# Optimization experiments

Hardware: AMD Instinct MI355X
Metric: run time of the kernel (lower is better)

The kernel has to match this reference:

```python
import jax, jax.numpy as jnp
import numpy as np

HIDDEN = 4096
NUM_HEADS = 32
NUM_KV_HEADS = 8
HEAD_DIM = HIDDEN // NUM_HEADS  # 128
Q_SIZE = NUM_HEADS * HEAD_DIM    # 4096
KV_SIZE = NUM_KV_HEADS * HEAD_DIM  # 1024
SCALE = 1.0 / HEAD_DIM  # attention_multiplier=None -> head_dim ** (-1)
ROPE_BASE = 10000.0


def _rope_neox(x, positions):
    # x: [B, S, H, D], positions: [B, S] int
    half = HEAD_DIM // 2
    inv_freq = 1.0 / (ROPE_BASE ** (jnp.arange(0, half, dtype=jnp.float32) / half))
    freqs = positions.astype(jnp.float32)[..., None] * inv_freq  # [B, S, half]
    cos = jnp.cos(freqs)[:, :, None, :]  # [B, S, 1, half]
    sin = jnp.sin(freqs)[:, :, None, :]
    x1, x2 = x[..., :half], x[..., half:]
    return jnp.concatenate([x1 * cos - x2 * sin, x2 * cos + x1 * sin], axis=-1)


def setup_inputs() -> dict:
    key = jax.random.key(0)
    k1, k2, k3 = jax.random.split(key, 3)
    B, S = 2, 2048
    positions = jnp.broadcast_to(jnp.arange(S, dtype=jnp.int32), (B, S))
    hidden_states = jax.random.normal(k1, (B, S, HIDDEN), dtype=jnp.float32) * 0.02
    w_qkv = jax.random.normal(k2, (Q_SIZE + 2 * KV_SIZE, HIDDEN), dtype=jnp.float32) * 0.02
    w_o = jax.random.normal(k3, (HIDDEN, Q_SIZE), dtype=jnp.float32) * 0.02
    return {"positions": positions, "hidden_states": hidden_states, "w_qkv": w_qkv, "w_o": w_o}


def reference(positions, hidden_states, w_qkv, w_o):
    B, S, _ = hidden_states.shape
    # fused QKV projection
    qkv = jnp.einsum('bsh,oh->bso', hidden_states, w_qkv)
    q = qkv[..., :Q_SIZE].reshape(B, S, NUM_HEADS, HEAD_DIM)
    k = qkv[..., Q_SIZE:Q_SIZE + KV_SIZE].reshape(B, S, NUM_KV_HEADS, HEAD_DIM)
    v = qkv[..., Q_SIZE + KV_SIZE:].reshape(B, S, NUM_KV_HEADS, HEAD_DIM)
    # neox-style RoPE on q and k
    q = _rope_neox(q, positions)
    k = _rope_neox(k, positions)
    # GQA: repeat kv heads
    rep = NUM_HEADS // NUM_KV_HEADS
    k = jnp.repeat(k, rep, axis=2)  # [B, S, NUM_HEADS, D]
    v = jnp.repeat(v, rep, axis=2)
    # causal attention
    scores = jnp.einsum('bqhd,bkhd->bhqk', q, k) * SCALE
    causal = jnp.tril(jnp.ones((S, S), dtype=bool))
    scores = jnp.where(causal, scores, jnp.finfo(scores.dtype).min)
    probs = jax.nn.softmax(scores, axis=-1)
    attn = jnp.einsum('bhqk,bkhd->bqhd', probs, v).reshape(B, S, Q_SIZE)
    # output projection
    return jnp.einsum('bsq,hq->bsh', attn, w_o)
```

## Files before the change

kernel.cpp:

```cpp
#include <hip/hip_runtime.h>
#include <hip/hip_bf16.h>
#include <cmath>

typedef __bf16 bf16x8 __attribute__((ext_vector_type(8)));
typedef __bf16 bf16x4 __attribute__((ext_vector_type(4)));
typedef float  f32x4  __attribute__((ext_vector_type(4)));
typedef unsigned int u32;
typedef u32 u32x4 __attribute__((ext_vector_type(4)));

#define AS1 __attribute__((address_space(1)))
#define AS3 __attribute__((address_space(3)))
#define GLDS16(gp, lp) __builtin_amdgcn_global_load_lds((AS1 void*)(gp), (AS3 void*)(lp), 16, 0, 0)

#define B_DIM 2
#define S_LEN 2048
#define HIDDEN 4096
#define NHEADS 32
#define NKV 8
#define HDIM 128
#define QSZ 4096
#define KVSZ 1024
#define QKVSZ 6144
#define GK 4096
#define ATT_SCALE 0.0078125f
#define L2E 1.4426950408889634f

__global__ __launch_bounds__(256) void conv3_f32_bf16(const float* __restrict__ i0, __bf16* __restrict__ o0, int n0,
                                                      const float* __restrict__ i1, __bf16* __restrict__ o1, int n1,
                                                      const float* __restrict__ i2, __bf16* __restrict__ o2, int n2) {
    const int total = n0 + n1 + n2;
    for (int idx = blockIdx.x * 256 + threadIdx.x; idx < total; idx += gridDim.x * 256) {
        const float* in; __bf16* out; int j = idx;
        if (j < n0) { in = i0; out = o0; }
        else if ((j -= n0) < n1) { in = i1; out = o1; }
        else { j -= n1; in = i2; out = o2; }
        float4 v = ((const float4*)in)[j];
        bf16x4 o;
        o[0] = (__bf16)v.x; o[1] = (__bf16)v.y; o[2] = (__bf16)v.z; o[3] = (__bf16)v.w;
        ((bf16x4*)out)[j] = o;
    }
}

__global__ __launch_bounds__(256) void rope_table_kernel(float* __restrict__ ct,
                                                         float* __restrict__ st) {
    int idx = blockIdx.x * 256 + threadIdx.x;
    int p = idx >> 6, i = idx & 63;
    float inv = expf(-(float)i * (9.210340371976184f / 64.0f));
    float freq = (float)p * inv;
    float s, c;
    sincosf(freq, &s, &c);
    ct[idx] = c; st[idx] = s;
}

template<typename OUT, bool VDIR>
__global__ __launch_bounds__(512, 2) void gemm256(const __bf16* __restrict__ A,
                                                  const __bf16* __restrict__ B,
                                                  OUT* __restrict__ C,
                                                  __bf16* __restrict__ Vt,
                                                  int N) {
    __shared__ __bf16 Asm[2 * 16384 + 2 * 16384];
    char* Bbase = (char*)Asm + 65536;

    const int tid = threadIdx.x;
    const int w = tid >> 6, l = tid & 63;
    const int l15 = l & 15, l4 = l >> 4;
    const int wr = w >> 2, wc = w & 3;

    const int nwg = gridDim.x * gridDim.y;
    const int orig = blockIdx.y * gridDim.x + blockIdx.x;
    const int swz = (orig & 7) * (nwg >> 3) + (orig >> 3);
    const int bx = swz % gridDim.x, by = swz / gridDim.x;
    const int m0 = by * 256, n0 = bx * 256;

    const __bf16* Ag = A + (size_t)m0 * GK;
    const __bf16* Bg = B + (size_t)n0 * GK;

#define STAGE_AQ(q, tile) do {                                                  \
        int c_ = (q) * 512 + tid;                                               \
        int r_ = c_ >> 3;                                                       \
        int jg_ = (tid & 7) ^ (r_ & 7);                                         \
        GLDS16(Ag + (size_t)r_ * GK + (tile) * 64 + jg_ * 8,                    \
               (char*)Asm + ((tile) & 1) * 32768 + c_ * 16);                    \
    } while (0)
#define STAGE_BS(s, tile) do {                                                  \
        _Pragma("unroll")                                                       \
        for (int i_ = 0; i_ < 2; ++i_) {                                        \
            int v_ = i_ * 512 + tid;                                            \
            int r_ = (v_ >> 8) * 64 + (s) * 32 + ((v_ >> 3) & 31);              \
            int jg_ = (v_ & 7) ^ (r_ & 7);                                      \
            int c_ = r_ * 8 + (v_ & 7);                                         \
            GLDS16(Bg + (size_t)r_ * GK + (tile) * 64 + jg_ * 8,                \
                   Bbase + ((tile) & 1) * 32768 + c_ * 16);                     \
        }                                                                       \
    } while (0)

#define LOAD_A(DST, MH) do {                                                    \
        _Pragma("unroll")                                                       \
        for (int m2 = 0; m2 < 4; ++m2) {                                        \
            int row = wr * 128 + ((MH) * 4 + m2) * 16 + l15;                    \
            _Pragma("unroll")                                                   \
            for (int kk = 0; kk < 2; ++kk) {                                    \
                int j = (kk * 4 + l4) ^ (row & 7);                              \
                DST[m2][kk] = *(const bf16x8*)(Als + row * 64 + j * 8);         \
            }                                                                   \
        }                                                                       \
    } while (0)
#define LOAD_B(DST, NH) do {                                                    \
        _Pragma("unroll")                                                       \
        for (int n2 = 0; n2 < 2; ++n2) {                                        \
            int row = wc * 64 + ((NH) * 2 + n2) * 16 + l15;                     \
            _Pragma("unroll")                                                   \
            for (int kk = 0; kk < 2; ++kk) {                                    \
                int j = (kk * 4 + l4) ^ (row & 7);                              \
                DST[n2][kk] = *(const bf16x8*)(Bls + row * 64 + j * 8);         \
            }                                                                   \
        }                                                                       \
    } while (0)
#define MFMA_QUAD(AF, BF, MI0, NI0)                                             \
    _Pragma("unroll")                                                           \
    for (int m2 = 0; m2 < 4; ++m2)                                              \
        _Pragma("unroll")                                                       \
        for (int n2 = 0; n2 < 2; ++n2)                                          \
            _Pragma("unroll")                                                   \
            for (int kk = 0; kk < 2; ++kk)                                      \
                acc[(MI0) + m2][(NI0) + n2] =                                   \
                    __builtin_amdgcn_mfma_f32_16x16x32_bf16(                    \
                        AF[m2][kk], BF[n2][kk], acc[(MI0) + m2][(NI0) + n2], 0, 0, 0);

    f32x4 acc[8][4] = {};

    const int T = GK / 64;
    STAGE_AQ(0, 0); STAGE_AQ(1, 0); STAGE_AQ(2, 0); STAGE_AQ(3, 0);
    STAGE_BS(0, 0); STAGE_BS(1, 0);
    STAGE_AQ(0, 1); STAGE_AQ(2, 1); STAGE_BS(0, 1);
    asm volatile("s_waitcnt vmcnt(4)" ::: "memory");
    __builtin_amdgcn_s_barrier();

    for (int t = 0; t < T; ++t) {
        const __bf16* Als = Asm + (t & 1) * 16384;
        const __bf16* Bls = (__bf16*)Bbase + (t & 1) * 16384;
        bf16x8 af0[4][2], af1[4][2], bA[2][2], bB[2][2];
        LOAD_A(af0, 0);
        LOAD_B(bA, 0);
        if (t + 1 < T) { STAGE_AQ(1, t + 1); STAGE_AQ(3, t + 1); }
        __builtin_amdgcn_s_barrier();
        __builtin_amdgcn_s_setprio(1);
        MFMA_QUAD(af0, bA, 0, 0);
        __builtin_amdgcn_s_setprio(0);
        __builtin_amdgcn_s_barrier();
        LOAD_B(bB, 1);
        if (t + 1 < T) STAGE_BS(1, t + 1);
        __builtin_amdgcn_s_barrier();
        __builtin_amdgcn_s_setprio(1);
        MFMA_QUAD(af0, bB, 0, 2);
        __builtin_amdgcn_s_setprio(0);
        __builtin_amdgcn_s_barrier();
        LOAD_A(af1, 1);
        if (t + 2 < T) { STAGE_AQ(0, t + 2); STAGE_AQ(2, t + 2); }
        __builtin_amdgcn_s_barrier();
        __builtin_amdgcn_s_setprio(1);
        MFMA_QUAD(af1, bA, 4, 0);
        __builtin_amdgcn_s_setprio(0);
        __builtin_amdgcn_s_barrier();
        if (t + 2 < T) STAGE_BS(0, t + 2);
        __builtin_amdgcn_s_barrier();
        __builtin_amdgcn_s_setprio(1);
        MFMA_QUAD(af1, bB, 4, 2);
        __builtin_amdgcn_s_setprio(0);
        if (t + 2 < T)      { asm volatile("s_waitcnt vmcnt(4)" ::: "memory"); }
        else if (t + 1 < T) { asm volatile("s_waitcnt vmcnt(0)" ::: "memory"); }
        __builtin_amdgcn_s_barrier();
    }
#undef MFMA_QUAD
#undef LOAD_A
#undef LOAD_B
#undef STAGE_AQ
#undef STAGE_BS

    if (VDIR && n0 >= QSZ + KVSZ) {
#pragma unroll
        for (int mi = 0; mi < 8; ++mi) {
            int s0 = m0 + wr * 128 + mi * 16 + l4 * 4;
            int b = s0 >> 11, s = s0 & 2047;
#pragma unroll
            for (int ni = 0; ni < 4; ++ni) {
                int vcol = n0 - (QSZ + KVSZ) + wc * 64 + ni * 16 + l15;
                int g = vcol >> 7, d = vcol & 127;
                bf16x4 o4;
#pragma unroll
                for (int r = 0; r < 4; ++r) o4[r] = (__bf16)acc[mi][ni][r];
                *(bf16x4*)(Vt + ((size_t)((b * 8 + g) * HDIM + d)) * S_LEN + s) = o4;
            }
        }
    } else {
#pragma unroll
        for (int mi = 0; mi < 8; ++mi)
#pragma unroll
            for (int ni = 0; ni < 4; ++ni)
#pragma unroll
                for (int r = 0; r < 4; ++r)
                    C[(size_t)(m0 + wr * 128 + mi * 16 + l4 * 4 + r) * N
                      + n0 + wc * 64 + ni * 16 + l15] = (OUT)acc[mi][ni][r];
    }
}

__global__ __launch_bounds__(256) void rope_kernel(const __bf16* __restrict__ qkv,
                                                   const int* __restrict__ pos,
                                                   const float* __restrict__ ct,
                                                   const float* __restrict__ st,
                                                   __bf16* __restrict__ Qb,
                                                   __bf16* __restrict__ Kb) {
    const int tid = threadIdx.x;
    const int tok = blockIdx.x;
    const int b = tok >> 11, s = tok & 2047;
    const int p = pos[tok];
    const __bf16* base = qkv + (size_t)tok * QKVSZ;
    const float* cb = ct + (size_t)p * 64;
    const float* sb = st + (size_t)p * 64;
    for (int u = tid; u < 640; u += 256) {
        int head = u >> 4, i = (u & 15) * 4;
        float4 c4 = *(const float4*)(cb + i);
        float4 s4 = *(const float4*)(sb + i);
        const bool isQ = (head < 32);
        const __bf16* src = base + (isQ ? head * HDIM : QSZ + (head - 32) * HDIM);
        bf16x4 x1 = *(const bf16x4*)(src + i);
        bf16x4 x2 = *(const bf16x4*)(src + 64 + i);
        float c[4] = {c4.x, c4.y, c4.z, c4.w};
        float sn[4] = {s4.x, s4.y, s4.z, s4.w};
        bf16x4 o1, o2;
        if (isQ) {
#pragma unroll
            for (int k = 0; k < 4; ++k) {
                float a = (float)x1[k], bv = (float)x2[k];
                o1[k] = (__bf16)((a * c[k] - bv * sn[k]) * ATT_SCALE);
                o2[k] = (__bf16)((bv * c[k] + a * sn[k]) * ATT_SCALE);
            }
            size_t o = ((size_t)(b * 32 + head) * S_LEN + s) * HDIM + i;
            *(bf16x4*)(Qb + o)      = o1;
            *(bf16x4*)(Qb + o + 64) = o2;
        } else {
#pragma unroll
            for (int k = 0; k < 4; ++k) {
                float a = (float)x1[k], bv = (float)x2[k];
                o1[k] = (__bf16)(a * c[k] - bv * sn[k]);
                o2[k] = (__bf16)(bv * c[k] + a * sn[k]);
            }
            int g = head - 32;
            size_t o = ((size_t)(b * 8 + g) * S_LEN + s) * HDIM + i;
            *(bf16x4*)(Kb + o)      = o1;
            *(bf16x4*)(Kb + o + 64) = o2;
        }
    }
}

__global__ __launch_bounds__(512, 2) void attn_kernel(const __bf16* __restrict__ Q,
                                                      const __bf16* __restrict__ K,
                                                      const __bf16* __restrict__ Vt,
                                                      __bf16* __restrict__ O) {
    const int tid = threadIdx.x;
    const int w = tid >> 6, l = tid & 63;
    const int l15 = l & 15, l4 = l >> 4;
    const int flat = blockIdx.x + (blockIdx.y << 2) + (blockIdx.z << 7);
    const int swz = (flat & 7) * 32 + (flat >> 3);
    const int p = swz & 3;
    const int hb = swz >> 2;
    const int h = hb & 31, b = hb >> 5;
    const int g = h >> 2;

    __shared__ __bf16 Ks[4][64 * 128];
    __shared__ __bf16 Vs[4][128 * 64];

    const __bf16* Kp = K + (size_t)(b * 8 + g) * S_LEN * HDIM;
    const __bf16* Vp = Vt + (size_t)(b * 8 + g) * HDIM * S_LEN;

#define RED16(x, OPINS) do {                                                      \
        u32 ra_ = __builtin_bit_cast(u32, x), rb_;                                \
        asm("v_mov_b32 %0, %1" : "=v"(rb_) : "v"(ra_));                           \
        asm("v_permlane16_swap_b32 %0, %1" : "+v"(ra_), "+v"(rb_));               \
        x = OPINS(__builtin_bit_cast(float, ra_), __builtin_bit_cast(float, rb_));\
    } while (0)
#define RED32(x, OPINS) do {                                                      \
        u32 ra_ = __builtin_bit_cast(u32, x), rb_;                                \
        asm("v_mov_b32 %0, %1" : "=v"(rb_) : "v"(ra_));                           \
        asm("v_permlane32_swap_b32 %0, %1" : "+v"(ra_), "+v"(rb_));               \
        x = OPINS(__builtin_bit_cast(float, ra_), __builtin_bit_cast(float, rb_));\
    } while (0)
#define FADD_(a_, b_) ((a_) + (b_))

#define STAGE(ktile) do {                                                          \
        const int buf_ = (ktile) & 3;                                              \
        const __bf16* kbase = Kp + (size_t)(ktile) * 64 * HDIM;                    \
        _Pragma("unroll")                                                          \
        for (int i_ = 0; i_ < 2; ++i_) {                                           \
            int c_ = i_ * 512 + tid;                \
            int row_ = c_ >> 4, cc_ = (c_ & 15) ^ (row_ & 7);                      \
            GLDS16(kbase + (size_t)row_ * HDIM + cc_ * 8,                          \
                   (char*)Ks[buf_] + c_ * 16);                                     \
        }                                                                          \
        const __bf16* vbase = Vp + (size_t)(ktile) * 64;                           \
        _Pragma("unroll")                                                          \
        for (int i_ = 0; i_ < 2; ++i_) {                                           \
            int c_ = i_ * 512 + tid;                \
            int row_ = c_ >> 3, cc_ = (c_ & 7) ^ (row_ & 7);                       \
            GLDS16(vbase + (size_t)row_ * S_LEN + cc_ * 8,                         \
                   (char*)Vs[buf_] + c_ * 16);                                     \
        }                                                                          \
    } while (0)

    for (int pi = 0; pi < 2; ++pi) {
        const int qt = pi ? (7 - p) : p;
        const int qw0 = qt * 256 + w * 32;
        const __bf16* Qp = Q + ((size_t)((b * 32 + h) * S_LEN + qw0)) * HDIM;

        bf16x8 qf[2][4];
#pragma unroll
        for (int qh = 0; qh < 2; ++qh)
#pragma unroll
            for (int kk = 0; kk < 4; ++kk)
                qf[qh][kk] = *(const bf16x8*)(Qp + (size_t)(qh * 16 + l15) * HDIM + kk * 32 + l4 * 8);

        f32x4 acc[2][8] = {};
        float m[2]    = {-1e30f, -1e30f};
        float lsum[2] = {0.f, 0.f};

        const int nkt = 4 * qt + 4;
        if (pi) { asm volatile("s_waitcnt vmcnt(0)" ::: "memory"); }
        STAGE(0);
        STAGE(1);
        STAGE(2);

        for (int kt = 0; kt < nkt; ++kt) {
            if (kt + 3 < nkt) STAGE(kt + 3);
            {
                int rem = nkt - 1 - kt;
                if (rem >= 3)      { asm volatile("s_waitcnt vmcnt(12)" ::: "memory"); }
                else if (rem == 2) { asm volatile("s_waitcnt vmcnt(8)"  ::: "memory"); }
                else if (rem == 1) { asm volatile("s_waitcnt vmcnt(4)"  ::: "memory"); }
                else               { asm volatile("s_waitcnt vmcnt(0)"  ::: "memory"); }
            }
            __builtin_amdgcn_sched_barrier(0);
            __builtin_amdgcn_s_barrier();
            __builtin_amdgcn_sched_barrier(0);
            const int cur = kt & 3;
            if (kt * 64 <= qw0 + 31) {
                f32x4 sfr[2][4];
                __builtin_amdgcn_s_setprio(1);
#pragma unroll
                for (int fn = 0; fn < 4; ++fn) {
                    f32x4 sa0 = {}, sa1 = {};
#pragma unroll
                    for (int kk = 0; kk < 4; ++kk) {
                        int row = fn * 16 + l15;
                        int cc = (kk * 4 + l4) ^ (l15 & 7);
                        bf16x8 kb = *(const bf16x8*)(Ks[cur] + row * HDIM + cc * 8);
                        sa0 = __builtin_amdgcn_mfma_f32_16x16x32_bf16(kb, qf[0][kk], sa0, 0, 0, 0);
                        sa1 = __builtin_amdgcn_mfma_f32_16x16x32_bf16(kb, qf[1][kk], sa1, 0, 0, 0);
                    }
                    sfr[0][fn] = sa0; sfr[1][fn] = sa1;
                }
                __builtin_amdgcn_s_setprio(0);
                const bool needmask = (kt * 64 + 63 > qw0);
                bf16x8 pb[2][2];
#pragma unroll
                for (int qh = 0; qh < 2; ++qh) {
                    const int qrow = qw0 + qh * 16 + l15;
                    float pmax = -1e30f;
#pragma unroll
                    for (int fn = 0; fn < 4; ++fn)
#pragma unroll
                        for (int r = 0; r < 4; ++r) {
                            float v = sfr[qh][fn][r];
                            if (needmask) {
                                int kcol = kt * 64 + fn * 16 + l4 * 4 + r;
                                if (kcol > qrow) v = -1e30f;
                            }
                            sfr[qh][fn][r] = v;
                            pmax = fmaxf(pmax, v);
                        }
                    RED16(pmax, fmaxf);
                    RED32(pmax, fmaxf);
                    if (!__all(pmax - m[qh] <= 8.0f)) {
                        float mn = fmaxf(m[qh], pmax);
                        float alpha = exp2f((m[qh] - mn) * L2E);
                        m[qh] = mn;
                        lsum[qh] *= alpha;
#pragma unroll
                        for (int n = 0; n < 8; ++n)
#pragma unroll
                            for (int r = 0; r < 4; ++r) acc[qh][n][r] *= alpha;
                    }
                    float rs = 0.f;
                    u32 pk01[4], pk23[4];
#pragma unroll
                    for (int fn = 0; fn < 4; ++fn) {
                        float p0 = exp2f((sfr[qh][fn][0] - m[qh]) * L2E);
                        float p1 = exp2f((sfr[qh][fn][1] - m[qh]) * L2E);
                        float p2 = exp2f((sfr[qh][fn][2] - m[qh]) * L2E);
                        float p3 = exp2f((sfr[qh][fn][3] - m[qh]) * L2E);
                        rs += (p0 + p1) + (p2 + p3);
                        asm("v_cvt_pk_bf16_f32 %0, %1, %2" : "=v"(pk01[fn]) : "v"(p0), "v"(p1));
                        asm("v_cvt_pk_bf16_f32 %0, %1, %2" : "=v"(pk23[fn]) : "v"(p2), "v"(p3));
                    }
                    RED16(rs, FADD_);
                    RED32(rs, FADD_);
                    lsum[qh] += rs;
#pragma unroll
                    for (int kk = 0; kk < 2; ++kk) {
                        u32 w0 = pk01[2 * kk], w2 = pk01[2 * kk + 1];
                        asm("v_permlane32_swap_b32 %0, %1" : "+v"(w0), "+v"(w2));
                        asm("v_permlane16_swap_b32 %0, %1" : "+v"(w0), "+v"(w2));
                        u32 w1 = pk23[2 * kk], w3 = pk23[2 * kk + 1];
                        asm("v_permlane32_swap_b32 %0, %1" : "+v"(w1), "+v"(w3));
                        asm("v_permlane16_swap_b32 %0, %1" : "+v"(w1), "+v"(w3));
                        u32x4 wv;
                        wv[0] = w0; wv[1] = w1; wv[2] = w2; wv[3] = w3;
                        pb[qh][kk] = __builtin_bit_cast(bf16x8, wv);
                    }
                }
                __builtin_amdgcn_s_setprio(1);
#pragma unroll
                for (int kk = 0; kk < 2; ++kk) {
#pragma unroll
                    for (int n = 0; n < 8; ++n) {
                        int row = n * 16 + l15;
                        int cc = (kk * 4 + l4) ^ (l15 & 7);
                        bf16x8 vb = *(const bf16x8*)(Vs[cur] + row * 64 + cc * 8);
                        acc[0][n] = __builtin_amdgcn_mfma_f32_16x16x32_bf16(vb, pb[0][kk], acc[0][n], 0, 0, 0);
                        acc[1][n] = __builtin_amdgcn_mfma_f32_16x16x32_bf16(vb, pb[1][kk], acc[1][n], 0, 0, 0);
                    }
                }
                __builtin_amdgcn_s_setprio(0);
            }
            __builtin_amdgcn_sched_barrier(0);
            __builtin_amdgcn_s_barrier();
            __builtin_amdgcn_sched_barrier(0);
        }
#pragma unroll
        for (int qh = 0; qh < 2; ++qh) {
            float inv = 1.0f / lsum[qh];
            int qrow = qw0 + qh * 16 + l15;
            __bf16* obase = O + ((size_t)(b * S_LEN) + qrow) * QSZ + h * HDIM + l4 * 4;
#pragma unroll
            for (int n = 0; n < 8; ++n) {
                bf16x4 o4;
#pragma unroll
                for (int r = 0; r < 4; ++r) o4[r] = (__bf16)(acc[qh][n][r] * inv);
                *(bf16x4*)(obase + n * 16) = o4;
            }
        }
    }
#undef STAGE
#undef RED16
#undef RED32
#undef FADD_
}

extern "C" void kernel_launch(void* const* d_in, const int* in_sizes, int n_in,
                              void* d_out, int out_size, void* d_ws, size_t ws_size,
                              hipStream_t stream) {
    const int*   pos    = (const int*)d_in[0];
    const float* hidden = (const float*)d_in[1];
    const float* wqkv   = (const float*)d_in[2];
    const float* wo     = (const float*)d_in[3];
    float* out = (float*)d_out;

    __bf16* hb    = (__bf16*)d_ws;
    __bf16* wqb   = hb  + 16777216;
    __bf16* wob   = wqb + 25165824;
    __bf16* qkv   = wob + 16777216;
    __bf16* Qb    = qkv + 25165824;
    __bf16* Kb    = Qb  + 16777216;
    __bf16* Vtb   = Kb  + 4194304;
    __bf16* attnb = Vtb + 4194304;
    float*  rc    = (float*)(attnb + 16777216);
    float*  rs    = rc + 131072;

    conv3_f32_bf16<<<2048, 256, 0, stream>>>(hidden, hb, 4194304,
                                             wqkv, wqb, 6291456,
                                             wo, wob, 4194304);
    rope_table_kernel<<<512, 256, 0, stream>>>(rc, rs);
    gemm256<__bf16, true><<<dim3(QKVSZ / 256, (B_DIM * S_LEN) / 256), 512, 0, stream>>>(
        hb, wqb, qkv, Vtb, QKVSZ);
    rope_kernel<<<B_DIM * S_LEN, 256, 0, stream>>>(qkv, pos, rc, rs, Qb, Kb);
    attn_kernel<<<dim3(4, NHEADS, B_DIM), 512, 0, stream>>>(Qb, Kb, Vtb, attnb);
    gemm256<float, false><<<dim3(HIDDEN / 256, (B_DIM * S_LEN) / 256), 512, 0, stream>>>(
        attnb, wob, out, nullptr, HIDDEN);
}
```

Measured before the change: 515.0 us.

## Fuse RoPE into QKV GEMM epilogue via LDS staging, drop separate rope kernel

The QKV GEMM epilogue now stages the Q/K output tile through shared memory as bf16, then applies neox RoPE (with attention scale for Q) and writes directly to the head-major Q and K buffers. The standalone rope kernel and the intermediate qkv buffer are removed. This avoids a kernel launch and a full write-then-read of the QKV activations. In exchange the GEMM epilogue gets extra LDS traffic and barriers plus gathered cos/sin table loads.

```diff
diff --git a/kernel.cpp b/kernel.cpp
--- a/kernel.cpp
+++ b/kernel.cpp
@@ -52,11 +52,16 @@
     ct[idx] = c; st[idx] = s;
 }
 
-template<typename OUT, bool VDIR>
+template<typename OUT, int MODE>
 __global__ __launch_bounds__(512, 2) void gemm256(const __bf16* __restrict__ A,
                                                   const __bf16* __restrict__ B,
                                                   OUT* __restrict__ C,
                                                   __bf16* __restrict__ Vt,
+                                                  __bf16* __restrict__ Qb,
+                                                  __bf16* __restrict__ Kb,
+                                                  const int* __restrict__ pos,
+                                                  const float* __restrict__ ct,
+                                                  const float* __restrict__ st,
                                                   int N) {
     __shared__ __bf16 Asm[2 * 16384 + 2 * 16384];
     char* Bbase = (char*)Asm + 65536;
@@ -177,19 +182,74 @@
 #undef STAGE_AQ
 #undef STAGE_BS
 
-    if (VDIR && n0 >= QSZ + KVSZ) {
-#pragma unroll
-        for (int mi = 0; mi < 8; ++mi) {
-            int s0 = m0 + wr * 128 + mi * 16 + l4 * 4;
-            int b = s0 >> 11, s = s0 & 2047;
-#pragma unroll
-            for (int ni = 0; ni < 4; ++ni) {
-                int vcol = n0 - (QSZ + KVSZ) + wc * 64 + ni * 16 + l15;
-                int g = vcol >> 7, d = vcol & 127;
-                bf16x4 o4;
-#pragma unroll
-                for (int r = 0; r < 4; ++r) o4[r] = (__bf16)acc[mi][ni][r];
-                *(bf16x4*)(Vt + ((size_t)((b * 8 + g) * HDIM + d)) * S_LEN + s) = o4;
+    if (MODE == 1) {
+        if (n0 >= QSZ + KVSZ) {
+#pragma unroll
+            for (int mi = 0; mi < 8; ++mi) {
+                int s0 = m0 + wr * 128 + mi * 16 + l4 * 4;
+                int b = s0 >> 11, s = s0 & 2047;
+#pragma unroll
+                for (int ni = 0; ni < 4; ++ni) {
+                    int vcol = n0 - (QSZ + KVSZ) + wc * 64 + ni * 16 + l15;
+                    int g = vcol >> 7, d = vcol & 127;
+                    bf16x4 o4;
+#pragma unroll
+                    for (int r = 0; r < 4; ++r) o4[r] = (__bf16)acc[mi][ni][r];
+                    *(bf16x4*)(Vt + ((size_t)((b * 8 + g) * HDIM + d)) * S_LEN + s) = o4;
+                }
+            }
+        } else {
+            __bf16* X = (__bf16*)Asm;
+            __syncthreads();
+#pragma unroll
+            for (int mi = 0; mi < 8; ++mi)
+#pragma unroll
+                for (int ni = 0; ni < 4; ++ni)
+#pragma unroll
+                    for (int r = 0; r < 4; ++r)
+                        X[(wr * 128 + mi * 16 + l4 * 4 + r) * 256
+                          + wc * 64 + ni * 16 + l15] = (__bf16)acc[mi][ni][r];
+            __syncthreads();
+            const bool isQ = (n0 < QSZ);
+#pragma unroll
+            for (int it = 0; it < 16; ++it) {
+                int idx = it * 512 + tid;
+                int q4 = (idx & 15) * 4;
+                int hh = (idx >> 4) & 1;
+                int lt = idx >> 5;
+                int tok = m0 + lt;
+                int bb = tok >> 11, ss = tok & 2047;
+                int pp = pos[tok];
+                float4 c4 = *(const float4*)(ct + (size_t)pp * 64 + q4);
+                float4 s4 = *(const float4*)(st + (size_t)pp * 64 + q4);
+                bf16x4 x1 = *(const bf16x4*)(X + lt * 256 + hh * 128 + q4);
+                bf16x4 x2 = *(const bf16x4*)(X + lt * 256 + hh * 128 + 64 + q4);
+                float cc[4] = {c4.x, c4.y, c4.z, c4.w};
+                float sn[4] = {s4.x, s4.y, s4.z, s4.w};
+                bf16x4 o1, o2;
+                if (isQ) {
+#pragma unroll
+                    for (int k = 0; k < 4; ++k) {
+                        float a = (float)x1[k], bv = (float)x2[k];
+                        o1[k] = (__bf16)((a * cc[k] - bv * sn[k]) * ATT_SCALE);
+                        o2[k] = (__bf16)((bv * cc[k] + a * sn[k]) * ATT_SCALE);
+                    }
+                    int gh = (n0 >> 7) + hh;
+                    size_t o = ((size_t)(bb * 32 + gh) * S_LEN + ss) * HDIM + q4;
+                    *(bf16x4*)(Qb + o)      = o1;
+                    *(bf16x4*)(Qb + o + 64) = o2;
+                } else {
+#pragma unroll
+                    for (int k = 0; k < 4; ++k) {
+                        float a = (float)x1[k], bv = (float)x2[k];
+                        o1[k] = (__bf16)(a * cc[k] - bv * sn[k]);
+                        o2[k] = (__bf16)(bv * cc[k] + a * sn[k]);
+                    }
+                    int gk = ((n0 - QSZ) >> 7) + hh;
+                    size_t o = ((size_t)(bb * 8 + gk) * S_LEN + ss) * HDIM + q4;
+                    *(bf16x4*)(Kb + o)      = o1;
+                    *(bf16x4*)(Kb + o + 64) = o2;
+                }
             }
         }
     } else {
@@ -201,55 +261,6 @@
                 for (int r = 0; r < 4; ++r)
                     C[(size_t)(m0 + wr * 128 + mi * 16 + l4 * 4 + r) * N
                       + n0 + wc * 64 + ni * 16 + l15] = (OUT)acc[mi][ni][r];
-    }
-}
-
-__global__ __launch_bounds__(256) void rope_kernel(const __bf16* __restrict__ qkv,
-                                                   const int* __restrict__ pos,
-                                                   const float* __restrict__ ct,
-                                                   const float* __restrict__ st,
-                                                   __bf16* __restrict__ Qb,
-                                                   __bf16* __restrict__ Kb) {
-    const int tid = threadIdx.x;
-    const int tok = blockIdx.x;
-    const int b = tok >> 11, s = tok & 2047;
-    const int p = pos[tok];
-    const __bf16* base = qkv + (size_t)tok * QKVSZ;
-    const float* cb = ct + (size_t)p * 64;
-    const float* sb = st + (size_t)p * 64;
-    for (int u = tid; u < 640; u += 256) {
-        int head = u >> 4, i = (u & 15) * 4;
-        float4 c4 = *(const float4*)(cb + i);
-        float4 s4 = *(const float4*)(sb + i);
-        const bool isQ = (head < 32);
-        const __bf16* src = base + (isQ ? head * HDIM : QSZ + (head - 32) * HDIM);
-        bf16x4 x1 = *(const bf16x4*)(src + i);
-        bf16x4 x2 = *(const bf16x4*)(src + 64 + i);
-        float c[4] = {c4.x, c4.y, c4.z, c4.w};
-        float sn[4] = {s4.x, s4.y, s4.z, s4.w};
-        bf16x4 o1, o2;
-        if (isQ) {
-#pragma unroll
-            for (int k = 0; k < 4; ++k) {
-                float a = (float)x1[k], bv = (float)x2[k];
-                o1[k] = (__bf16)((a * c[k] - bv * sn[k]) * ATT_SCALE);
-                o2[k] = (__bf16)((bv * c[k] + a * sn[k]) * ATT_SCALE);
-            }
-            size_t o = ((size_t)(b * 32 + head) * S_LEN + s) * HDIM + i;
-            *(bf16x4*)(Qb + o)      = o1;
-            *(bf16x4*)(Qb + o + 64) = o2;
-        } else {
-#pragma unroll
-            for (int k = 0; k < 4; ++k) {
-                float a = (float)x1[k], bv = (float)x2[k];
-                o1[k] = (__bf16)(a * c[k] - bv * sn[k]);
-                o2[k] = (__bf16)(bv * c[k] + a * sn[k]);
-            }
-            int g = head - 32;
-            size_t o = ((size_t)(b * 8 + g) * S_LEN + s) * HDIM + i;
-            *(bf16x4*)(Kb + o)      = o1;
-            *(bf16x4*)(Kb + o + 64) = o2;
-        }
     }
 }
 
@@ -467,8 +478,7 @@
     __bf16* hb    = (__bf16*)d_ws;
     __bf16* wqb   = hb  + 16777216;
     __bf16* wob   = wqb + 25165824;
-    __bf16* qkv   = wob + 16777216;
-    __bf16* Qb    = qkv + 25165824;
+    __bf16* Qb    = wob + 16777216;
     __bf16* Kb    = Qb  + 16777216;
     __bf16* Vtb   = Kb  + 4194304;
     __bf16* attnb = Vtb + 4194304;
@@ -479,10 +489,9 @@
                                              wqkv, wqb, 6291456,
                                              wo, wob, 4194304);
     rope_table_kernel<<<512, 256, 0, stream>>>(rc, rs);
-    gemm256<__bf16, true><<<dim3(QKVSZ / 256, (B_DIM * S_LEN) / 256), 512, 0, stream>>>(
-        hb, wqb, qkv, Vtb, QKVSZ);
-    rope_kernel<<<B_DIM * S_LEN, 256, 0, stream>>>(qkv, pos, rc, rs, Qb, Kb);
+    gemm256<__bf16, 1><<<dim3(QKVSZ / 256, (B_DIM * S_LEN) / 256), 512, 0, stream>>>(
+        hb, wqb, ((__bf16*)nullptr), Vtb, Qb, Kb, pos, rc, rs, QKVSZ);
     attn_kernel<<<dim3(4, NHEADS, B_DIM), 512, 0, stream>>>(Qb, Kb, Vtb, attnb);
-    gemm256<float, false><<<dim3(HIDDEN / 256, (B_DIM * S_LEN) / 256), 512, 0, stream>>>(
-        attnb, wob, out, nullptr, HIDDEN);
+    gemm256<float, 0><<<dim3(HIDDEN / 256, (B_DIM * S_LEN) / 256), 512, 0, stream>>>(
+        attnb, wob, out, nullptr, nullptr, nullptr, nullptr, nullptr, nullptr, HIDDEN);
 }
```

Result: faster. 504.8 us (-2.0%).
